# Performance work log

Hardware: AMD Instinct MI355X
Metric: run time of the kernel (lower is better)

Reference implementation:

```python
import jax, jax.numpy as jnp
import numpy as np

D_MODEL = 1024
N_TILES = 16
N_CLASSES = 1024
BATCH = 65536
THRESH = 0.3  # ternary quantization threshold


def setup_inputs() -> dict:
    key = jax.random.key(0)
    k_x, k_s, k_w, k_b = jax.random.split(key, 4)
    x = jax.random.normal(k_x, (BATCH, D_MODEL), dtype=jnp.float32)
    # signatures_raw: n_tiles params of shape [d_model], init randn*0.5
    sigs_raw = jax.random.normal(k_s, (N_TILES, D_MODEL), dtype=jnp.float32) * 0.5
    # per-tile Linear(d_model, n_classes): weight [n_classes, d_model], bias [n_classes]
    lim = 1.0 / np.sqrt(D_MODEL)
    W = jax.random.uniform(k_w, (N_TILES, N_CLASSES, D_MODEL), dtype=jnp.float32, minval=-lim, maxval=lim)
    b = jax.random.uniform(k_b, (N_TILES, N_CLASSES), dtype=jnp.float32, minval=-lim, maxval=lim)
    return {"x": x, "sigs_raw": sigs_raw, "W": W, "b": b}


def _quantize_ternary(s):
    # straight-through ternary: forward = {-1, 0, +1}, backward = identity
    q = jnp.where(s > THRESH, 1.0, jnp.where(s < -THRESH, -1.0, 0.0)).astype(s.dtype)
    return s + jax.lax.stop_gradient(q - s)


def reference(x, sigs_raw, W, b):
    sigs = _quantize_ternary(sigs_raw)           # [T, D]
    scores = x @ sigs.T                          # [B, T]
    tile_indices = jnp.argmax(scores, axis=-1)   # [B]
    n_tiles = W.shape[0]
    logits = jnp.zeros((x.shape[0], W.shape[1]), dtype=x.dtype)  # [B, C]
    # fixed small loop over tiles (experts); select per-token result via mask
    for t in range(n_tiles):
        out_t = x @ W[t].T + b[t]                # [B, C]
        logits = jnp.where((tile_indices == t)[:, None], out_t, logits)
    return logits, tile_indices
```

## Files before the change

kernel.cpp:

```cpp
#include <hip/hip_runtime.h>
#include <hip/hip_bf16.h>
#include <stdint.h>

#define B_TOK 65536
#define DM 1024
#define NC 1024
#define NT 16
#define GAPTHR 0.25f

typedef __attribute__((ext_vector_type(4))) float f32x4;
typedef __attribute__((ext_vector_type(4))) unsigned int u32x4;
typedef __attribute__((ext_vector_type(4))) unsigned short u16x4;
typedef __attribute__((ext_vector_type(8))) short short8;

#define AS1(p) ((__attribute__((address_space(1))) void*)(p))
#define AS3(p) ((__attribute__((address_space(3))) void*)(p))

static __device__ inline unsigned short f2bf(float f) {
  __hip_bfloat16 h = __float2bfloat16(f);
  unsigned short u;
  __builtin_memcpy(&u, &h, 2);
  return u;
}

__global__ void k_prep(const float* __restrict__ sigs, unsigned int* __restrict__ mask,
                       unsigned short* __restrict__ Sb) {
  int d = threadIdx.x;
  unsigned int m = 0;
#pragma unroll
  for (int t = 0; t < NT; ++t) {
    float s = sigs[t * DM + d];
    float q = (s > 0.3f) ? 1.0f : ((s < -0.3f) ? -1.0f : 0.0f);
    if (s > 0.3f) m |= 1u << t;
    else if (s < -0.3f) m |= 1u << (16 + t);
    Sb[t * DM + d] = f2bf(q);
  }
  mask[d] = m;
}

__global__ __launch_bounds__(256) void k_pre(const float* __restrict__ x,
    const unsigned short* __restrict__ Sb, unsigned short* __restrict__ xb,
    int* __restrict__ tidx, float* __restrict__ oidx,
    int* __restrict__ fixlist, int* __restrict__ nfix, int* __restrict__ counts,
    const float* __restrict__ W, unsigned short* __restrict__ Wb)
{
  int bid = blockIdx.x;
  int tid = threadIdx.x;
  if (bid >= 1024) {
    const f32x4* W4 = (const f32x4*)W;
    u16x4* O = (u16x4*)Wb;
    int n4 = NT * NC * DM / 4;
    for (int i = (bid - 1024) * 256 + tid; i < n4; i += 512 * 256) {
      f32x4 v = W4[i];
      u16x4 o;
#pragma unroll
      for (int j = 0; j < 4; ++j) o[j] = f2bf(v[j]);
      O[i] = o;
    }
    return;
  }
  __shared__ int hist[16];
  if (tid < 16) hist[tid] = 0;
  __syncthreads();

  int w = tid >> 6, l = tid & 63;
  int lr = l & 15, lg = l >> 4;
  int tok0 = bid * 64 + w * 16;

  const float* xr = x + (size_t)(tok0 + lr) * DM + lg * 8;
  unsigned short* xbr = xb + (size_t)(tok0 + lr) * DM + lg * 8;
  const unsigned short* sr = Sb + (size_t)lr * DM + lg * 8;

  f32x4 accA = (f32x4){0.f, 0.f, 0.f, 0.f};
  f32x4 accB = (f32x4){0.f, 0.f, 0.f, 0.f};
  for (int kc = 0; kc < 32; kc += 2) {
    f32x4 v0 = *(const f32x4*)(xr + kc * 32);
    f32x4 v1 = *(const f32x4*)(xr + kc * 32 + 4);
    f32x4 v2 = *(const f32x4*)(xr + kc * 32 + 32);
    f32x4 v3 = *(const f32x4*)(xr + kc * 32 + 36);
    short8 a0, a1;
#pragma unroll
    for (int j = 0; j < 4; ++j) {
      a0[j]     = (short)f2bf(v0[j]);
      a0[4 + j] = (short)f2bf(v1[j]);
      a1[j]     = (short)f2bf(v2[j]);
      a1[4 + j] = (short)f2bf(v3[j]);
    }
    *(short8*)(xbr + kc * 32) = a0;
    *(short8*)(xbr + kc * 32 + 32) = a1;
    short8 b0 = *(const short8*)(sr + kc * 32);
    short8 b1 = *(const short8*)(sr + kc * 32 + 32);
    accA = __builtin_amdgcn_mfma_f32_16x16x32_bf16(a0, b0, accA, 0, 0, 0);
    accB = __builtin_amdgcn_mfma_f32_16x16x32_bf16(a1, b1, accB, 0, 0, 0);
  }
  f32x4 acc;
#pragma unroll
  for (int i = 0; i < 4; ++i) acc[i] = accA[i] + accB[i];

  float m1[4], m2v[4]; int i1[4];
#pragma unroll
  for (int i = 0; i < 4; ++i) { m1[i] = acc[i]; i1[i] = lr; m2v[i] = -1e30f; }
#pragma unroll
  for (int off = 1; off < 16; off <<= 1) {
#pragma unroll
    for (int i = 0; i < 4; ++i) {
      float bm  = __shfl_xor(m1[i], off);
      int   bi  = __shfl_xor(i1[i], off);
      float bm2 = __shfl_xor(m2v[i], off);
      bool bwin = (bm > m1[i]) || (bm == m1[i] && bi < i1[i]);
      float loser = bwin ? m1[i] : bm;
      m2v[i] = fmaxf(fmaxf(m2v[i], bm2), loser);
      if (bwin) { m1[i] = bm; i1[i] = bi; }
    }
  }
  if (lr == 0) {
#pragma unroll
    for (int i = 0; i < 4; ++i) {
      int tok = tok0 + lg * 4 + i;
      tidx[tok] = i1[i];
      oidx[tok] = (float)i1[i];
      atomicAdd(&hist[i1[i]], 1);
      if (m1[i] - m2v[i] < GAPTHR) {
        int p = atomicAdd(nfix, 1);
        fixlist[p] = tok;
      }
    }
  }
  __syncthreads();
  if (tid < 16 && hist[tid]) atomicAdd(&counts[tid], hist[tid]);
}

__global__ __launch_bounds__(256) void k_fix(const float* __restrict__ x,
    const unsigned int* __restrict__ mask, const int* __restrict__ fixlist,
    const int* __restrict__ nfix, int* __restrict__ tidx, float* __restrict__ oidx,
    int* __restrict__ counts)
{
  int n = *nfix;
  int l = threadIdx.x & 63;
  int gw = (blockIdx.x * 256 + threadIdx.x) >> 6;
  int nw = (gridDim.x * 256) >> 6;
  int t = l & 15, seg = l >> 4;

  for (int i = gw; i < n; i += nw) {
    int tok = fixlist[i];
    const float* xr = x + (size_t)tok * DM + seg * 256;
    const unsigned int* mr = mask + seg * 256;
    double acc0 = 0.0, acc1 = 0.0;
    for (int j = 0; j < 256; j += 4) {
      f32x4 xv = *(const f32x4*)(xr + j);
      u32x4 mv = *(const u32x4*)(mr + j);
#pragma unroll
      for (int u = 0; u < 4; ++u) {
        double c = ((mv[u] >> t) & 1u) ? (double)xv[u]
                 : (((mv[u] >> (16 + t)) & 1u) ? -(double)xv[u] : 0.0);
        if (u & 1) acc1 += c; else acc0 += c;
      }
    }
    double s = acc0 + acc1;
    s += __shfl_xor(s, 16);
    s += __shfl_xor(s, 32);
    double bv = s; int bi = t;
#pragma unroll
    for (int off = 1; off < 16; off <<= 1) {
      double ov = __shfl_xor(bv, off);
      int   oi = __shfl_xor(bi, off);
      if (ov > bv || (ov == bv && oi < bi)) { bv = ov; bi = oi; }
    }
    if (l == 0) {
      int old = tidx[tok];
      if (bi != old) {
        tidx[tok] = bi;
        oidx[tok] = (float)bi;
        atomicSub(&counts[old], 1);
        atomicAdd(&counts[bi], 1);
      }
    }
  }
}

__global__ void k_scan(const int* __restrict__ counts, int* __restrict__ offs) {
  if (threadIdx.x == 0) {
    int s = 0;
    for (int t = 0; t < NT; ++t) {
      offs[t] = s;
      s += (counts[t] + 255) & ~255;
    }
    offs[NT] = s;
  }
}

__global__ __launch_bounds__(256) void k_place(const int* __restrict__ tidx, const int* __restrict__ offs,
                                               int* __restrict__ cursor, int* __restrict__ perm) {
  __shared__ int h[16], base[16];
  int tid = threadIdx.x;
  if (tid < 16) h[tid] = 0;
  __syncthreads();
  int tok = blockIdx.x * 256 + tid;
  int t = tidx[tok];
  int myloc = atomicAdd(&h[t], 1);
  __syncthreads();
  if (tid < 16 && h[tid]) base[tid] = atomicAdd(&cursor[tid], h[tid]);
  __syncthreads();
  perm[offs[t] + base[t] + myloc] = tok;
}

__global__ __launch_bounds__(512, 2) void k_gemm(const unsigned short* __restrict__ xb,
    const unsigned short* __restrict__ Wb, const float* __restrict__ bias,
    const int* __restrict__ perm, const int* __restrict__ offs, float* __restrict__ out)
{
  __shared__ unsigned short lds[4][2][256 * 32];
  int bid0 = blockIdx.x;
  int bid = (bid0 & 7) * 136 + (bid0 >> 3);
  int mb = bid >> 2, nb = bid & 3;
  int total = offs[NT];
  int m0 = mb << 8;
  if (m0 >= total) return;
  int t = 0;
#pragma unroll
  for (int tt = 0; tt < NT; ++tt) if (m0 >= offs[tt + 1]) t = tt + 1;
  int c0 = nb << 8;
  int tid = threadIdx.x;

  int srow = tid >> 2;
  int kg = (((tid & 3) ^ ((tid >> 3) & 3)) << 3);
  int tkA0 = perm[m0 + srow];        if (tkA0 < 0) tkA0 = 0;
  int tkA1 = perm[m0 + 128 + srow];  if (tkA1 < 0) tkA1 = 0;
  const unsigned short* pA0 = xb + (size_t)tkA0 * DM + kg;
  const unsigned short* pA1 = xb + (size_t)tkA1 * DM + kg;
  const unsigned short* gWt = Wb + (size_t)t * NC * DM;
  const unsigned short* pB0 = gWt + (size_t)(c0 + srow) * DM + kg;
  const unsigned short* pB1 = gWt + (size_t)(c0 + 128 + srow) * DM + kg;

  f32x4 acc[8][4];
#pragma unroll
  for (int m = 0; m < 8; ++m)
#pragma unroll
    for (int n = 0; n < 4; ++n) acc[m][n] = (f32x4){0.f, 0.f, 0.f, 0.f};

  int wid = tid >> 6, l = tid & 63;
  int wr = wid >> 2, wc = wid & 3;
  int lr = l & 15, lk = l >> 4;
  int wr128 = wr * 128, wc64 = wc * 64;
  int goff = ((lk ^ ((lr >> 1) & 3)) << 3);

#define GLDS(g, lp) __builtin_amdgcn_global_load_lds(AS1(g), AS3(lp), 16, 0, 0)
#define STAGE_A(SS, KT) { \
  GLDS(pA0 + (KT) * 32, &lds[SS][0][tid * 8]); \
  GLDS(pA1 + (KT) * 32, &lds[SS][0][(512 + tid) * 8]); }
#define STAGE_B(SS, KT) { \
  GLDS(pB0 + (KT) * 32, &lds[SS][1][tid * 8]); \
  GLDS(pB1 + (KT) * 32, &lds[SS][1][(512 + tid) * 8]); }
#define RD_A(SLOT, M) (*(const short8*)&lds[SLOT][0][(wr128 + (M) * 16 + lr) * 32 + goff])
#define RD_B(SLOT, N) (*(const short8*)&lds[SLOT][1][(wc64 + (N) * 16 + lr) * 32 + goff])
#define MF(M_, N_, AV, BV) acc[M_][N_] = __builtin_amdgcn_mfma_f32_16x16x32_bf16(AV, BV, acc[M_][N_], 0, 0, 0)
#define MFMA4(M_, AV) { MF(M_, 0, AV, b0); MF(M_, 1, AV, b1); MF(M_, 2, AV, b2); MF(M_, 3, AV, b3); }
#define VM8() asm volatile("s_waitcnt vmcnt(8)" ::: "memory")
#define VM4() asm volatile("s_waitcnt vmcnt(4)" ::: "memory")
#define VM0() asm volatile("s_waitcnt vmcnt(0)" ::: "memory")

#define KTILE(KT, SLOT, SS, DOSTAGE, VMW) { \
  short8 b0 = RD_B(SLOT, 0), b1 = RD_B(SLOT, 1), b2 = RD_B(SLOT, 2), b3 = RD_B(SLOT, 3); \
  short8 a0 = RD_A(SLOT, 0), a1 = RD_A(SLOT, 1); \
  if (DOSTAGE) STAGE_A(SS, (KT) + 3); \
  __builtin_amdgcn_s_setprio(1); \
  MFMA4(0, a0); MFMA4(1, a1); \
  { short8 a2 = RD_A(SLOT, 2), a3 = RD_A(SLOT, 3); \
    MFMA4(2, a2); MFMA4(3, a3); } \
  { short8 a4 = RD_A(SLOT, 4), a5 = RD_A(SLOT, 5); \
    if (DOSTAGE) STAGE_B(SS, (KT) + 3); \
    MFMA4(4, a4); MFMA4(5, a5); } \
  { short8 a6 = RD_A(SLOT, 6), a7 = RD_A(SLOT, 7); \
    MFMA4(6, a6); MFMA4(7, a7); } \
  __builtin_amdgcn_s_setprio(0); \
  VMW; \
  __builtin_amdgcn_s_barrier(); }

  STAGE_A(0, 0); STAGE_B(0, 0);
  STAGE_A(1, 1); STAGE_B(1, 1);
  STAGE_A(2, 2); STAGE_B(2, 2);
  VM8();
  __builtin_amdgcn_s_barrier();

#pragma unroll 1
  for (int kt = 0; kt < 28; kt += 4) {
    KTILE(kt + 0, 0, 3, 1, VM8());
    KTILE(kt + 1, 1, 0, 1, VM8());
    KTILE(kt + 2, 2, 1, 1, VM8());
    KTILE(kt + 3, 3, 2, 1, VM8());
  }
  KTILE(28, 0, 3, 1, VM8());
  KTILE(29, 1, 0, 0, VM4());
  KTILE(30, 2, 1, 0, VM0());
  KTILE(31, 3, 2, 0, ((void)0));

  float bv[4];
#pragma unroll
  for (int n = 0; n < 4; ++n) bv[n] = bias[t * NC + c0 + wc64 + n * 16 + lr];
#pragma unroll
  for (int m = 0; m < 8; ++m) {
#pragma unroll
    for (int j = 0; j < 4; ++j) {
      int prow = m0 + wr128 + m * 16 + lk * 4 + j;
      int tok = perm[prow];
      if (tok >= 0) {
#pragma unroll
        for (int n = 0; n < 4; ++n)
          out[(size_t)tok * NC + c0 + wc64 + n * 16 + lr] = acc[m][n][j] + bv[n];
      }
    }
  }
}

extern "C" void kernel_launch(void* const* d_in, const int* in_sizes, int n_in,
                              void* d_out, int out_size, void* d_ws, size_t ws_size,
                              hipStream_t stream) {
  const float* x    = (const float*)d_in[0];
  const float* sigs = (const float*)d_in[1];
  const float* W    = (const float*)d_in[2];
  const float* bias = (const float*)d_in[3];
  float* out = (float*)d_out;
  float* oidx = out + (size_t)B_TOK * NC;

  char* ws = (char*)d_ws;
  unsigned short* xb   = (unsigned short*)ws;
  unsigned short* Wb   = (unsigned short*)(ws + 134217728);
  int* perm            = (int*)(ws + 167772160);
  int* tidx            = (int*)(ws + 168050688);
  unsigned int* mask   = (unsigned int*)(ws + 168312832);
  unsigned short* Sb   = (unsigned short*)(ws + 168316928);
  int* fixlist         = (int*)(ws + 168349696);
  int* ctrl            = (int*)(ws + 168611840);
  int* counts = ctrl;
  int* cursor = ctrl + 16;
  int* offs   = ctrl + 32;
  int* nfix   = ctrl + 49;

  hipMemsetAsync(perm, 0xFF, 278528, stream);
  hipMemsetAsync(ctrl, 0, 256, stream);

  k_prep<<<1, 1024, 0, stream>>>(sigs, mask, Sb);
  k_pre<<<1536, 256, 0, stream>>>(x, Sb, xb, tidx, oidx, fixlist, nfix, counts, W, Wb);
  k_fix<<<512, 256, 0, stream>>>(x, mask, fixlist, nfix, tidx, oidx, counts);
  k_scan<<<1, 64, 0, stream>>>(counts, offs);
  k_place<<<256, 256, 0, stream>>>(tidx, offs, cursor, perm);
  k_gemm<<<dim3(272 * 4), 512, 0, stream>>>(xb, Wb, bias, perm, offs, out);
}
```

Measured before the change: 353.5 us.

## Shrink GEMM tile to 256x128 with 3-stage LDS pipeline for higher occupancy

The grouped GEMM tile is cut from 256x256 to 256x128 columns. The grid doubles to 272*8 blocks and the per-wave accumulators halve. The LDS pipeline goes from 4 to 3 stages and prefetches 2 k-tiles ahead, with launch bounds raised to allow 4 blocks per CU. The aim is more resident waves to hide latency, at the cost of lower arithmetic intensity, since each A row is reloaded for twice as many column blocks.

```diff
diff --git a/kernel.cpp b/kernel.cpp
--- a/kernel.cpp
+++ b/kernel.cpp
@@ -204,21 +204,21 @@
   perm[offs[t] + base[t] + myloc] = tok;
 }
 
-__global__ __launch_bounds__(512, 2) void k_gemm(const unsigned short* __restrict__ xb,
+__global__ __launch_bounds__(512, 4) void k_gemm(const unsigned short* __restrict__ xb,
     const unsigned short* __restrict__ Wb, const float* __restrict__ bias,
     const int* __restrict__ perm, const int* __restrict__ offs, float* __restrict__ out)
 {
-  __shared__ unsigned short lds[4][2][256 * 32];
+  __shared__ unsigned short lds[3][384 * 32];
   int bid0 = blockIdx.x;
-  int bid = (bid0 & 7) * 136 + (bid0 >> 3);
-  int mb = bid >> 2, nb = bid & 3;
+  int bid = (bid0 & 7) * 272 + (bid0 >> 3);
+  int mb = bid >> 3, nb = bid & 7;
   int total = offs[NT];
   int m0 = mb << 8;
   if (m0 >= total) return;
   int t = 0;
 #pragma unroll
   for (int tt = 0; tt < NT; ++tt) if (m0 >= offs[tt + 1]) t = tt + 1;
-  int c0 = nb << 8;
+  int c0 = nb << 7;
   int tid = threadIdx.x;
 
   int srow = tid >> 2;
@@ -227,80 +227,71 @@
   int tkA1 = perm[m0 + 128 + srow];  if (tkA1 < 0) tkA1 = 0;
   const unsigned short* pA0 = xb + (size_t)tkA0 * DM + kg;
   const unsigned short* pA1 = xb + (size_t)tkA1 * DM + kg;
-  const unsigned short* gWt = Wb + (size_t)t * NC * DM;
-  const unsigned short* pB0 = gWt + (size_t)(c0 + srow) * DM + kg;
-  const unsigned short* pB1 = gWt + (size_t)(c0 + 128 + srow) * DM + kg;
-
-  f32x4 acc[8][4];
-#pragma unroll
-  for (int m = 0; m < 8; ++m)
+  const unsigned short* pB  = Wb + (size_t)t * NC * DM + (size_t)(c0 + srow) * DM + kg;
+  int sA0 = srow * 32 + (tid & 3) * 8;
+  int sA1 = (128 + srow) * 32 + (tid & 3) * 8;
+  int sB  = (256 + srow) * 32 + (tid & 3) * 8;
+
+  f32x4 acc[4][4];
+#pragma unroll
+  for (int m = 0; m < 4; ++m)
 #pragma unroll
     for (int n = 0; n < 4; ++n) acc[m][n] = (f32x4){0.f, 0.f, 0.f, 0.f};
 
   int wid = tid >> 6, l = tid & 63;
-  int wr = wid >> 2, wc = wid & 3;
+  int wr = wid >> 1, wc = wid & 1;
   int lr = l & 15, lk = l >> 4;
-  int wr128 = wr * 128, wc64 = wc * 64;
+  int wr64 = wr * 64, wc64 = wc * 64;
   int goff = ((lk ^ ((lr >> 1) & 3)) << 3);
 
 #define GLDS(g, lp) __builtin_amdgcn_global_load_lds(AS1(g), AS3(lp), 16, 0, 0)
-#define STAGE_A(SS, KT) { \
-  GLDS(pA0 + (KT) * 32, &lds[SS][0][tid * 8]); \
-  GLDS(pA1 + (KT) * 32, &lds[SS][0][(512 + tid) * 8]); }
-#define STAGE_B(SS, KT) { \
-  GLDS(pB0 + (KT) * 32, &lds[SS][1][tid * 8]); \
-  GLDS(pB1 + (KT) * 32, &lds[SS][1][(512 + tid) * 8]); }
-#define RD_A(SLOT, M) (*(const short8*)&lds[SLOT][0][(wr128 + (M) * 16 + lr) * 32 + goff])
-#define RD_B(SLOT, N) (*(const short8*)&lds[SLOT][1][(wc64 + (N) * 16 + lr) * 32 + goff])
+#define STAGE_A0(SS, KT) GLDS(pA0 + (KT) * 32, &lds[SS][sA0])
+#define STAGE_A1(SS, KT) GLDS(pA1 + (KT) * 32, &lds[SS][sA1])
+#define STAGE_Bx(SS, KT) GLDS(pB  + (KT) * 32, &lds[SS][sB])
+#define RD_A(SLOT, M) (*(const short8*)&lds[SLOT][(wr64 + (M) * 16 + lr) * 32 + goff])
+#define RD_B(SLOT, N) (*(const short8*)&lds[SLOT][8192 + (wc64 + (N) * 16 + lr) * 32 + goff])
 #define MF(M_, N_, AV, BV) acc[M_][N_] = __builtin_amdgcn_mfma_f32_16x16x32_bf16(AV, BV, acc[M_][N_], 0, 0, 0)
 #define MFMA4(M_, AV) { MF(M_, 0, AV, b0); MF(M_, 1, AV, b1); MF(M_, 2, AV, b2); MF(M_, 3, AV, b3); }
-#define VM8() asm volatile("s_waitcnt vmcnt(8)" ::: "memory")
-#define VM4() asm volatile("s_waitcnt vmcnt(4)" ::: "memory")
+#define VM3() asm volatile("s_waitcnt vmcnt(3)" ::: "memory")
 #define VM0() asm volatile("s_waitcnt vmcnt(0)" ::: "memory")
 
 #define KTILE(KT, SLOT, SS, DOSTAGE, VMW) { \
   short8 b0 = RD_B(SLOT, 0), b1 = RD_B(SLOT, 1), b2 = RD_B(SLOT, 2), b3 = RD_B(SLOT, 3); \
   short8 a0 = RD_A(SLOT, 0), a1 = RD_A(SLOT, 1); \
-  if (DOSTAGE) STAGE_A(SS, (KT) + 3); \
+  if (DOSTAGE) STAGE_A0(SS, (KT) + 2); \
   __builtin_amdgcn_s_setprio(1); \
   MFMA4(0, a0); MFMA4(1, a1); \
   { short8 a2 = RD_A(SLOT, 2), a3 = RD_A(SLOT, 3); \
-    MFMA4(2, a2); MFMA4(3, a3); } \
-  { short8 a4 = RD_A(SLOT, 4), a5 = RD_A(SLOT, 5); \
-    if (DOSTAGE) STAGE_B(SS, (KT) + 3); \
-    MFMA4(4, a4); MFMA4(5, a5); } \
-  { short8 a6 = RD_A(SLOT, 6), a7 = RD_A(SLOT, 7); \
-    MFMA4(6, a6); MFMA4(7, a7); } \
+    if (DOSTAGE) STAGE_A1(SS, (KT) + 2); \
+    MFMA4(2, a2); \
+    if (DOSTAGE) STAGE_Bx(SS, (KT) + 2); \
+    MFMA4(3, a3); } \
   __builtin_amdgcn_s_setprio(0); \
   VMW; \
   __builtin_amdgcn_s_barrier(); }
 
-  STAGE_A(0, 0); STAGE_B(0, 0);
-  STAGE_A(1, 1); STAGE_B(1, 1);
-  STAGE_A(2, 2); STAGE_B(2, 2);
-  VM8();
+  STAGE_A0(0, 0); STAGE_A1(0, 0); STAGE_Bx(0, 0);
+  STAGE_A0(1, 1); STAGE_A1(1, 1); STAGE_Bx(1, 1);
+  VM3();
   __builtin_amdgcn_s_barrier();
 
 #pragma unroll 1
-  for (int kt = 0; kt < 28; kt += 4) {
-    KTILE(kt + 0, 0, 3, 1, VM8());
-    KTILE(kt + 1, 1, 0, 1, VM8());
-    KTILE(kt + 2, 2, 1, 1, VM8());
-    KTILE(kt + 3, 3, 2, 1, VM8());
-  }
-  KTILE(28, 0, 3, 1, VM8());
-  KTILE(29, 1, 0, 0, VM4());
-  KTILE(30, 2, 1, 0, VM0());
-  KTILE(31, 3, 2, 0, ((void)0));
+  for (int kt = 0; kt < 30; kt += 3) {
+    KTILE(kt + 0, 0, 2, 1, VM3());
+    KTILE(kt + 1, 1, 0, 1, VM3());
+    KTILE(kt + 2, 2, 1, 1, VM3());
+  }
+  KTILE(30, 0, 2, 0, VM0());
+  KTILE(31, 1, 0, 0, ((void)0));
 
   float bv[4];
 #pragma unroll
   for (int n = 0; n < 4; ++n) bv[n] = bias[t * NC + c0 + wc64 + n * 16 + lr];
 #pragma unroll
-  for (int m = 0; m < 8; ++m) {
+  for (int m = 0; m < 4; ++m) {
 #pragma unroll
     for (int j = 0; j < 4; ++j) {
-      int prow = m0 + wr128 + m * 16 + lk * 4 + j;
+      int prow = m0 + wr64 + m * 16 + lk * 4 + j;
       int tok = perm[prow];
       if (tok >= 0) {
 #pragma unroll
@@ -343,5 +334,5 @@
   k_fix<<<512, 256, 0, stream>>>(x, mask, fixlist, nfix, tidx, oidx, counts);
   k_scan<<<1, 64, 0, stream>>>(counts, offs);
   k_place<<<256, 256, 0, stream>>>(tidx, offs, cursor, perm);
-  k_gemm<<<dim3(272 * 4), 512, 0, stream>>>(xb, Wb, bias, perm, offs, out);
-}
+  k_gemm<<<dim3(272 * 8), 512, 0, stream>>>(xb, Wb, bias, perm, offs, out);
+}
```

New measurement: 386.0 us. +9.2%, slower.
